# Kernel tuning notes

Hardware: AMD Instinct MI355X
Metric: run time of the kernel (lower is better)

## Reference

```python
import jax, jax.numpy as jnp
import numpy as np

HIDDEN, N_HEADS, HEAD_DIM, CACHE_LEN, BATCH = 4096, 32, 128, 512, 32


def setup_inputs() -> dict:
    key = jax.random.key(0)
    ks = jax.random.split(key, 7)
    s = 0.02
    return {
        "x": jax.random.normal(ks[0], (BATCH, 1, HIDDEN), jnp.float32),
        "k_cache": jax.random.normal(ks[1], (BATCH, N_HEADS, CACHE_LEN, HEAD_DIM), jnp.float32),
        "v_cache": jax.random.normal(ks[2], (BATCH, N_HEADS, CACHE_LEN, HEAD_DIM), jnp.float32),
        # torch nn.Linear weights: (out_features, in_features), y = x @ W.T
        "wq": jax.random.normal(ks[3], (N_HEADS * HEAD_DIM, HIDDEN), jnp.float32) * s,
        "wk": jax.random.normal(ks[4], (N_HEADS * HEAD_DIM, HIDDEN), jnp.float32) * s,
        "wv": jax.random.normal(ks[5], (N_HEADS * HEAD_DIM, HIDDEN), jnp.float32) * s,
        "wo": jax.random.normal(ks[6], (HIDDEN, N_HEADS * HEAD_DIM), jnp.float32) * s,
    }


def reference(x, k_cache, v_cache, wq, wk, wv, wo):
    bsz = x.shape[0]
    # projections: (b, 1, H*D) -> (b, n_heads, 1, head_dim)
    def proj(w):
        return (x @ w.T).reshape(bsz, 1, N_HEADS, HEAD_DIM).transpose(0, 2, 1, 3)
    q, k_new, v_new = proj(wq), proj(wk), proj(wv)
    scale = 1.0 / HEAD_DIM ** 0.5
    # cache attention: (b, h, 1, cache_len)
    cache_scores = jnp.einsum("bhqd,bhkd->bhqk", q, k_cache) * scale
    cache_probs = jax.nn.softmax(cache_scores, axis=-1)
    cache_out = jnp.einsum("bhqk,bhkd->bhqd", cache_probs, v_cache)
    # new-token attention: softmax over a single key (probs == 1), kept faithful
    new_scores = jnp.einsum("bhqd,bhkd->bhqk", q, k_new) * scale
    new_probs = jax.nn.softmax(new_scores, axis=-1)
    new_out = jnp.einsum("bhqk,bhkd->bhqd", new_probs, v_new)
    out = cache_out + new_out  # note: sum of two separately-normalized softmaxes (as in source)
    out = out.transpose(0, 2, 1, 3).reshape(bsz, 1, N_HEADS * HEAD_DIM)
    return out @ wo.T
```

## Files before the change

kernel.cpp:

```cpp
#include <hip/hip_runtime.h>
#include <hip/hip_bf16.h>

#define HIDDEN 4096
#define NHEADS 32
#define HDIM 128
#define CLEN 512
#define BATCH 32

__device__ __forceinline__ void proj_body(const float* __restrict__ X,
                                          const float* __restrict__ W,
                                          float* __restrict__ Y,
                                          int rowblock) {
    const int t   = threadIdx.x;
    const int l   = t & 63;
    const int wid = t >> 6;
    const int rowbase = rowblock * 8;
    const float* wp = W + (size_t)rowbase * HIDDEN + 4 * l;
    const float* xp = X + (size_t)(wid * 4) * HIDDEN + 4 * l;

    float v[32];
    #pragma unroll
    for (int j = 0; j < 32; ++j) v[j] = 0.f;

    #pragma unroll 2
    for (int kp = 0; kp < HIDDEN; kp += 256) {
        float4 wv[8], xv[4];
        #pragma unroll
        for (int r = 0; r < 8; ++r)
            wv[r] = *(const float4*)(wp + (size_t)r * HIDDEN + kp);
        #pragma unroll
        for (int b = 0; b < 4; ++b)
            xv[b] = *(const float4*)(xp + (size_t)b * HIDDEN + kp);
        #pragma unroll
        for (int r = 0; r < 8; ++r) {
            #pragma unroll
            for (int b = 0; b < 4; ++b) {
                v[r * 4 + b] += wv[r].x * xv[b].x + wv[r].y * xv[b].y +
                                wv[r].z * xv[b].z + wv[r].w * xv[b].w;
            }
        }
    }

    #pragma unroll
    for (int j = 0; j < 32; ++j) v[j] += __shfl_xor(v[j], 1);
    #pragma unroll
    for (int s = 1; s <= 5; ++s) {
        const int m = 1 << s;
        const int bit = (l >> s) & 1;
        #pragma unroll
        for (int i = 0; i < (32 >> s); ++i) {
            float t0 = __shfl_xor(v[2 * i], m);
            float t1 = __shfl_xor(v[2 * i + 1], m);
            v[i] = bit ? (v[2 * i + 1] + t1) : (v[2 * i] + t0);
        }
    }
    if (!(l & 1)) {
        const int j = l >> 1;
        const int r = j >> 2, b = j & 3;
        Y[(size_t)(wid * 4 + b) * HIDDEN + rowbase + r] = v[0];
    }
}

__global__ __launch_bounds__(512, 2) void proj_dual_kernel(const float* __restrict__ X,
                                                           const float* __restrict__ Wa,
                                                           const float* __restrict__ Wb,
                                                           float* __restrict__ Ya,
                                                           float* __restrict__ Yb) {
    const int bx = blockIdx.x;
    proj_body(X, (bx & 1) ? Wb : Wa, (bx & 1) ? Yb : Ya, bx >> 1);
}

__global__ __launch_bounds__(512, 2) void proj_out_kernel(const float* __restrict__ X,
                                                          const float* __restrict__ W,
                                                          float* __restrict__ Y) {
    proj_body(X, W, Y, blockIdx.x);
}

#define PSTRIDE 17

__global__ __launch_bounds__(512, 4) void attn_kernel(const float* __restrict__ q,
                                                      const float* __restrict__ kc,
                                                      const float* __restrict__ vc,
                                                      const float* __restrict__ vnew,
                                                      float* __restrict__ attn_out) {
    __shared__ float part_lds[CLEN * PSTRIDE];
    __shared__ float sc[CLEN];
    __shared__ float red[16];
    __shared__ float part[8 * HDIM];
    const int t = threadIdx.x;
    const int w = t >> 6;
    const int l = t & 63;
    const int bh = blockIdx.x;
    const int b = bh >> 5, h = bh & 31;
    const float* K = kc + (size_t)bh * CLEN * HDIM;
    const float* V = vc + (size_t)bh * CLEN * HDIM;
    const float scale = 0.088388347648318447f;
    const int d0 = 4 * (l & 31);
    const int kh = l >> 5;
    const size_t hoff = (size_t)b * HIDDEN + h * HDIM;
    float4 q4 = *(const float4*)(q + hoff + d0);

    const int kbeg = w * 64;
    const bool wr = (l & 16) == 0;
    const int pj = l & 15;
    #pragma unroll 8
    for (int r = 0; r < 32; ++r) {
        const int k = kbeg + 2 * r + kh;
        float4 kv = *(const float4*)(K + (size_t)k * HDIM + d0);
        float p = q4.x * kv.x + q4.y * kv.y + q4.z * kv.z + q4.w * kv.w;
        p += __shfl_xor(p, 16);
        if (wr) part_lds[k * PSTRIDE + pj] = p;
    }
    __syncthreads();

    float s = 0.f;
    #pragma unroll
    for (int j = 0; j < 16; ++j) s += part_lds[t * PSTRIDE + j];
    s *= scale;
    float mx = s;
    #pragma unroll
    for (int m = 32; m; m >>= 1) mx = fmaxf(mx, __shfl_xor(mx, m));
    if (l == 0) red[w] = mx;
    __syncthreads();
    mx = fmaxf(fmaxf(fmaxf(red[0], red[1]), fmaxf(red[2], red[3])),
               fmaxf(fmaxf(red[4], red[5]), fmaxf(red[6], red[7])));
    float e = __expf(s - mx);
    sc[t] = e;
    float es = e;
    #pragma unroll
    for (int m = 32; m; m >>= 1) es += __shfl_xor(es, m);
    if (l == 0) red[8 + w] = es;
    __syncthreads();
    const float inv = 1.0f / (red[8] + red[9] + red[10] + red[11] +
                              red[12] + red[13] + red[14] + red[15]);

    float4 acc = make_float4(0.f, 0.f, 0.f, 0.f);
    #pragma unroll 8
    for (int k = kbeg; k < kbeg + 64; k += 2) {
        float4 v4 = *(const float4*)(V + (size_t)(k + kh) * HDIM + d0);
        float p = sc[k + kh];
        acc.x += p * v4.x; acc.y += p * v4.y;
        acc.z += p * v4.z; acc.w += p * v4.w;
    }
    acc.x += __shfl_xor(acc.x, 32);
    acc.y += __shfl_xor(acc.y, 32);
    acc.z += __shfl_xor(acc.z, 32);
    acc.w += __shfl_xor(acc.w, 32);
    if (l < 32) *(float4*)(&part[w * HDIM + d0]) = acc;
    __syncthreads();
    if (t < HDIM) {
        float r = 0.f;
        #pragma unroll
        for (int ww = 0; ww < 8; ++ww) r += part[ww * HDIM + t];
        attn_out[hoff + t] = r * inv + vnew[hoff + t];
    }
}

extern "C" void kernel_launch(void* const* d_in, const int* in_sizes, int n_in,
                              void* d_out, int out_size, void* d_ws, size_t ws_size,
                              hipStream_t stream) {
    (void)in_sizes; (void)n_in; (void)out_size; (void)ws_size;
    const float* x  = (const float*)d_in[0];
    const float* kc = (const float*)d_in[1];
    const float* vc = (const float*)d_in[2];
    const float* wq = (const float*)d_in[3];
    const float* wv = (const float*)d_in[5];
    const float* wo = (const float*)d_in[6];
    float* out = (float*)d_out;

    float* q    = (float*)d_ws;
    float* vnew = q + BATCH * HIDDEN;
    float* attn = vnew + BATCH * HIDDEN;

    proj_dual_kernel<<<2 * (HIDDEN / 8), 512, 0, stream>>>(x, wq, wv, q, vnew);
    attn_kernel<<<BATCH * NHEADS, 512, 0, stream>>>(q, kc, vc, vnew, attn);
    proj_out_kernel<<<HIDDEN / 8, 512, 0, stream>>>(attn, wo, out);
}
```

Before: 213.7 us.

## Split attention over cache halves with flash-decoding style combine kernel

Attention for each (batch, head) is now split across two 256-thread blocks, each covering half of the KV cache and writing a partial output, max and exp-sum. A new combine kernel rescales and merges the two halves and adds the new-token value. The score reduction is also changed from a padded LDS buffer to a full wave shuffle reduction. The aim is more, smaller blocks for better occupancy and latency hiding on the memory-bound cache read, at the cost of an extra kernel launch and workspace round trip.

```diff
diff --git a/kernel.cpp b/kernel.cpp
--- a/kernel.cpp
+++ b/kernel.cpp
@@ -76,67 +76,67 @@
     proj_body(X, W, Y, blockIdx.x);
 }
 
-#define PSTRIDE 17
-
-__global__ __launch_bounds__(512, 4) void attn_kernel(const float* __restrict__ q,
-                                                      const float* __restrict__ kc,
-                                                      const float* __restrict__ vc,
-                                                      const float* __restrict__ vnew,
-                                                      float* __restrict__ attn_out) {
-    __shared__ float part_lds[CLEN * PSTRIDE];
-    __shared__ float sc[CLEN];
-    __shared__ float red[16];
-    __shared__ float part[8 * HDIM];
+#define KB 256
+
+__global__ __launch_bounds__(256, 8) void attn_split_kernel(
+        const float* __restrict__ q,
+        const float* __restrict__ kc,
+        const float* __restrict__ vc,
+        float* __restrict__ o_half,
+        float* __restrict__ ms,
+        float* __restrict__ ss) {
+    __shared__ float sc[KB];
+    __shared__ float red[8];
+    __shared__ float part[4 * HDIM];
     const int t = threadIdx.x;
     const int w = t >> 6;
     const int l = t & 63;
-    const int bh = blockIdx.x;
+    const int bid = blockIdx.x;
+    const int bh = bid >> 1;
+    const int half = bid & 1;
     const int b = bh >> 5, h = bh & 31;
-    const float* K = kc + (size_t)bh * CLEN * HDIM;
-    const float* V = vc + (size_t)bh * CLEN * HDIM;
+    const int kbase = half * KB;
+    const float* K = kc + (size_t)bh * CLEN * HDIM + (size_t)kbase * HDIM;
+    const float* V = vc + (size_t)bh * CLEN * HDIM + (size_t)kbase * HDIM;
     const float scale = 0.088388347648318447f;
     const int d0 = 4 * (l & 31);
     const int kh = l >> 5;
-    const size_t hoff = (size_t)b * HIDDEN + h * HDIM;
-    float4 q4 = *(const float4*)(q + hoff + d0);
-
-    const int kbeg = w * 64;
-    const bool wr = (l & 16) == 0;
-    const int pj = l & 15;
+    float4 q4 = *(const float4*)(q + (size_t)b * HIDDEN + h * HDIM + d0);
+
+    const int kw = w * 64;
     #pragma unroll 8
     for (int r = 0; r < 32; ++r) {
-        const int k = kbeg + 2 * r + kh;
+        const int k = kw + 2 * r + kh;
         float4 kv = *(const float4*)(K + (size_t)k * HDIM + d0);
         float p = q4.x * kv.x + q4.y * kv.y + q4.z * kv.z + q4.w * kv.w;
-        p += __shfl_xor(p, 16);
-        if (wr) part_lds[k * PSTRIDE + pj] = p;
-    }
-    __syncthreads();
-
-    float s = 0.f;
-    #pragma unroll
-    for (int j = 0; j < 16; ++j) s += part_lds[t * PSTRIDE + j];
-    s *= scale;
+        #pragma unroll
+        for (int m = 16; m; m >>= 1) p += __shfl_xor(p, m);
+        if ((l & 31) == 0) sc[k] = p * scale;
+    }
+    __syncthreads();
+
+    float s = sc[t];
     float mx = s;
     #pragma unroll
     for (int m = 32; m; m >>= 1) mx = fmaxf(mx, __shfl_xor(mx, m));
     if (l == 0) red[w] = mx;
     __syncthreads();
-    mx = fmaxf(fmaxf(fmaxf(red[0], red[1]), fmaxf(red[2], red[3])),
-               fmaxf(fmaxf(red[4], red[5]), fmaxf(red[6], red[7])));
+    mx = fmaxf(fmaxf(red[0], red[1]), fmaxf(red[2], red[3]));
     float e = __expf(s - mx);
     sc[t] = e;
     float es = e;
     #pragma unroll
     for (int m = 32; m; m >>= 1) es += __shfl_xor(es, m);
-    if (l == 0) red[8 + w] = es;
-    __syncthreads();
-    const float inv = 1.0f / (red[8] + red[9] + red[10] + red[11] +
-                              red[12] + red[13] + red[14] + red[15]);
+    if (l == 0) red[4 + w] = es;
+    __syncthreads();
+    if (t == 0) {
+        ms[bid] = mx;
+        ss[bid] = red[4] + red[5] + red[6] + red[7];
+    }
 
     float4 acc = make_float4(0.f, 0.f, 0.f, 0.f);
     #pragma unroll 8
-    for (int k = kbeg; k < kbeg + 64; k += 2) {
+    for (int k = kw; k < kw + 64; k += 2) {
         float4 v4 = *(const float4*)(V + (size_t)(k + kh) * HDIM + d0);
         float p = sc[k + kh];
         acc.x += p * v4.x; acc.y += p * v4.y;
@@ -149,11 +149,30 @@
     if (l < 32) *(float4*)(&part[w * HDIM + d0]) = acc;
     __syncthreads();
     if (t < HDIM) {
-        float r = 0.f;
-        #pragma unroll
-        for (int ww = 0; ww < 8; ++ww) r += part[ww * HDIM + t];
-        attn_out[hoff + t] = r * inv + vnew[hoff + t];
-    }
+        float r = part[t] + part[HDIM + t] + part[2 * HDIM + t] + part[3 * HDIM + t];
+        o_half[(size_t)bid * HDIM + t] = r;
+    }
+}
+
+__global__ __launch_bounds__(256) void combine_kernel(
+        const float* __restrict__ o_half,
+        const float* __restrict__ ms,
+        const float* __restrict__ ss,
+        const float* __restrict__ vnew,
+        float* __restrict__ attn_out) {
+    const int t = threadIdx.x;
+    const int bh = blockIdx.x * 2 + (t >> 7);
+    const int d = t & 127;
+    const float m0 = ms[2 * bh], m1 = ms[2 * bh + 1];
+    const float s0 = ss[2 * bh], s1 = ss[2 * bh + 1];
+    const float M = fmaxf(m0, m1);
+    const float w0 = __expf(m0 - M), w1 = __expf(m1 - M);
+    const float inv = 1.0f / (s0 * w0 + s1 * w1);
+    const float o0 = o_half[(size_t)(2 * bh) * HDIM + d];
+    const float o1 = o_half[(size_t)(2 * bh + 1) * HDIM + d];
+    const int b = bh >> 5, h = bh & 31;
+    const size_t idx = (size_t)b * HIDDEN + h * HDIM + d;
+    attn_out[idx] = (o0 * w0 + o1 * w1) * inv + vnew[idx];
 }
 
 extern "C" void kernel_launch(void* const* d_in, const int* in_sizes, int n_in,
@@ -168,11 +187,15 @@
     const float* wo = (const float*)d_in[6];
     float* out = (float*)d_out;
 
-    float* q    = (float*)d_ws;
-    float* vnew = q + BATCH * HIDDEN;
-    float* attn = vnew + BATCH * HIDDEN;
+    float* q      = (float*)d_ws;
+    float* vnew   = q + BATCH * HIDDEN;
+    float* attn   = vnew + BATCH * HIDDEN;
+    float* o_half = attn + BATCH * HIDDEN;
+    float* ms     = o_half + 2 * BATCH * NHEADS * HDIM;
+    float* ss     = ms + 2 * BATCH * NHEADS;
 
     proj_dual_kernel<<<2 * (HIDDEN / 8), 512, 0, stream>>>(x, wq, wv, q, vnew);
-    attn_kernel<<<BATCH * NHEADS, 512, 0, stream>>>(q, kc, vc, vnew, attn);
+    attn_split_kernel<<<2 * BATCH * NHEADS, 256, 0, stream>>>(q, kc, vc, o_half, ms, ss);
+    combine_kernel<<<BATCH * NHEADS / 2, 256, 0, stream>>>(o_half, ms, ss, vnew, attn);
     proj_out_kernel<<<HIDDEN / 8, 512, 0, stream>>>(attn, wo, out);
 }
```

New measurement: 198.7 us. 1.08x faster.
